# Optimization experiments

Hardware: AMD Instinct MI355X
Metric: run time of the kernel (lower is better)

The kernel has to match this reference:

```python
import jax, jax.numpy as jnp
import numpy as np

N_HEADS = 16


def _rope(q, k, freq_cos, freq_sin):
    # q,k: [B,S,H,hd]; freqs: [S, hd//2]
    B, S, H, hd = q.shape
    qr, qi = q.reshape(B, S, H, hd // 2, 2)[..., 0], q.reshape(B, S, H, hd // 2, 2)[..., 1]
    kr, ki = k.reshape(B, S, H, hd // 2, 2)[..., 0], k.reshape(B, S, H, hd // 2, 2)[..., 1]
    fc = freq_cos[None, :, None, :]  # [1,S,1,hd//2]
    fs = freq_sin[None, :, None, :]
    q_out = jnp.stack([qr * fc - qi * fs, qr * fs + qi * fc], axis=-1).reshape(B, S, H, hd)
    k_out = jnp.stack([kr * fc - ki * fs, kr * fs + ki * fc], axis=-1).reshape(B, S, H, hd)
    return q_out, k_out


def setup_inputs() -> dict:
    key = jax.random.key(0)
    ks = jax.random.split(key, 7)
    B, S, D = 2, 2048, 2048
    hd = D // N_HEADS
    scale = 1.0 / np.sqrt(D)
    return {
        "x": jax.random.normal(ks[0], (B, S, D), dtype=jnp.float32),
        "freq_cos": jnp.cos(jax.random.normal(ks[1], (S, hd // 2), dtype=jnp.float32)),
        "freq_sin": jnp.sin(jax.random.normal(ks[2], (S, hd // 2), dtype=jnp.float32)),
        "wq": jax.random.normal(ks[3], (D, D), dtype=jnp.float32) * scale,
        "wk": jax.random.normal(ks[4], (D, D), dtype=jnp.float32) * scale,
        "wv": jax.random.normal(ks[5], (D, D), dtype=jnp.float32) * scale,
        "wo": jax.random.normal(ks[6], (D, D), dtype=jnp.float32) * scale,
    }


def reference(x, freq_cos, freq_sin, wq, wk, wv, wo):
    B, S, D = x.shape
    H = N_HEADS
    hd = D // H
    # torch nn.Linear(weight [out,in]): y = x @ W^T
    q = (x @ wq.T).reshape(B, S, H, hd)
    k = (x @ wk.T).reshape(B, S, H, hd)
    v = (x @ wv.T).reshape(B, S, H, hd)
    q, k = _rope(q, k, freq_cos, freq_sin)
    # [B,H,S,hd]
    q = q.transpose(0, 2, 1, 3)
    k = k.transpose(0, 2, 1, 3)
    v = v.transpose(0, 2, 1, 3)
    scores = jnp.einsum("bhqd,bhkd->bhqk", q, k) / jnp.sqrt(jnp.float32(hd))
    causal = jnp.triu(jnp.full((S, S), -jnp.inf, dtype=scores.dtype), k=1)
    scores = scores + causal[None, None, :, :]
    probs = jax.nn.softmax(scores, axis=-1)
    out = jnp.einsum("bhqk,bhkd->bhqd", probs, v)
    out = out.transpose(0, 2, 1, 3).reshape(B, S, D)
    return out @ wo.T
```

## Files before the change

kernel.cpp:

```cpp
#include <hip/hip_runtime.h>
#include <hip/hip_bf16.h>
#include <stdint.h>

typedef unsigned short u16;
typedef unsigned int   u32;

typedef __attribute__((ext_vector_type(8))) short bf16x8;
typedef __attribute__((ext_vector_type(4))) float f32x4;
typedef __attribute__((ext_vector_type(4))) float f4;
typedef __attribute__((ext_vector_type(4))) u16   u16x4;

#define GLOBAL_AS __attribute__((address_space(1)))
#define LDS_AS    __attribute__((address_space(3)))

#define QSCALE (0.088388347648318447f * 1.4426950408889634f)

__device__ __forceinline__ void gload_lds16(const void* gsrc, void* ldst) {
    __builtin_amdgcn_global_load_lds((GLOBAL_AS const u32*)gsrc,
                                     (LDS_AS u32*)ldst, 16, 0, 0);
}

__device__ __forceinline__ float b2f(u16 u) {
    union { u32 i; float f; } x; x.i = ((u32)u) << 16; return x.f;
}
__device__ __forceinline__ u16 f2b(float f) {
    u32 u = __builtin_bit_cast(u32, f);
    u = (u + 0x7fff + ((u >> 16) & 1)) >> 16;
    return (u16)u;
}
__device__ __forceinline__ u16 f2b_tr(float f) {
    return (u16)(__builtin_bit_cast(u32, f) >> 16);
}

__global__ __launch_bounds__(256) void f2bf_kernel(const float* __restrict__ in,
                                                   u16* __restrict__ out, int n4) {
    int i = blockIdx.x * blockDim.x + threadIdx.x;
    if (i >= n4) return;
    f4 v = ((const f4*)in)[i];
    u16x4 o;
    o[0] = f2b(v[0]); o[1] = f2b(v[1]); o[2] = f2b(v[2]); o[3] = f2b(v[3]);
    ((u16x4*)out)[i] = o;
}

__global__ __launch_bounds__(256) void rope_kernel(u16* __restrict__ qkv,
                                                   const float* __restrict__ fc,
                                                   const float* __restrict__ fs) {
    const int S = 2048;
    int idx = blockIdx.x * blockDim.x + threadIdx.x;
    const int p   = idx & 1023;
    const int row = idx >> 10;
    const int s   = row & (S - 1);
    const int i   = p & 63;
    const float c = fc[s * 64 + i], sn = fs[s * 64 + i];
    u16* qa = qkv + (size_t)row * 6144 + p * 2;
    u16* ka = qa + 2048;
    u32 qq = *(const u32*)qa;
    float qr = b2f((u16)(qq & 0xffff)), qi = b2f((u16)(qq >> 16));
    u32 kk = *(const u32*)ka;
    float kr = b2f((u16)(kk & 0xffff)), ki = b2f((u16)(kk >> 16));
    u16 e0 = f2b(qr * c - qi * sn), e1 = f2b(qr * sn + qi * c);
    *(u32*)qa = (u32)e0 | ((u32)e1 << 16);
    e0 = f2b(kr * c - ki * sn); e1 = f2b(kr * sn + ki * c);
    *(u32*)ka = (u32)e0 | ((u32)e1 << 16);
}

template<int OUT_MODE>
__global__ __launch_bounds__(512, 2)
void gemm_bt(const u16* __restrict__ A, const u16* __restrict__ B,
             void* __restrict__ Cptr, int M, int N, int Kdim) {
    __shared__ char lds[3][49152];
    const int t = threadIdx.x, l = t & 63, w = t >> 6;
    const int g = l >> 4, r16 = l & 15;

    const int nwg = gridDim.x * gridDim.y;
    const int id  = blockIdx.y * gridDim.x + blockIdx.x;
    const int swz = (id & 7) * (nwg >> 3) + (id >> 3);
    const int bx  = swz % gridDim.x, by = swz / gridDim.x;
    const int m0 = by * 256, n0 = bx * 128;
    const int wm = w >> 1, wn = w & 1;
    const int rA = wm * 64, rB = wn * 64;

    f32x4 acc[4][4];
#pragma unroll
    for (int i = 0; i < 4; i++)
#pragma unroll
        for (int j = 0; j < 4; j++) acc[i][j] = (f32x4){0.f, 0.f, 0.f, 0.f};

    const int nk = Kdim >> 6;

    auto stage = [&](int kt, int bi) {
        const int k0 = kt << 6;
#pragma unroll
        for (int q = 0; q < 4; q++) {
            const int o = q * 8192 + w * 1024 + l * 16;
            const int row = o >> 7;
            const int cb = (o & 127) ^ ((row & 7) << 4);
            gload_lds16(A + (size_t)(m0 + row) * Kdim + k0 + (cb >> 1),
                        &lds[bi][q * 8192 + w * 1024]);
        }
#pragma unroll
        for (int q = 0; q < 2; q++) {
            const int o = q * 8192 + w * 1024 + l * 16;
            const int row = o >> 7;
            const int cb = (o & 127) ^ ((row & 7) << 4);
            gload_lds16(B + (size_t)(n0 + row) * Kdim + k0 + (cb >> 1),
                        &lds[bi][32768 + q * 8192 + w * 1024]);
        }
    };

    stage(0, 0);
    stage(1, 1);

    for (int kt = 0; kt < nk; ++kt) {
        const int cur = kt % 3;
        __builtin_amdgcn_sched_barrier(0);
        __builtin_amdgcn_s_barrier();
        stage((kt + 2) % nk, (kt + 2) % 3);
        asm volatile("s_waitcnt vmcnt(12)" ::: "memory");
        __builtin_amdgcn_s_barrier();
        __builtin_amdgcn_sched_barrier(0);

        const char* Ab = lds[cur];
        const char* Bb = lds[cur] + 32768;
        bf16x8 af[2][4], bfr[2][4];
#pragma unroll
        for (int kk = 0; kk < 2; kk++)
#pragma unroll
            for (int i = 0; i < 4; i++) {
                const int rowa = rA + i * 16 + r16;
                const int cba = (kk * 64 + g * 16) ^ ((rowa & 7) << 4);
                af[kk][i] = *(const bf16x8*)(Ab + rowa * 128 + cba);
                const int rowb = rB + i * 16 + r16;
                const int cbb = (kk * 64 + g * 16) ^ ((rowb & 7) << 4);
                bfr[kk][i] = *(const bf16x8*)(Bb + rowb * 128 + cbb);
            }
#pragma unroll
        for (int kk = 0; kk < 2; kk++)
#pragma unroll
            for (int mi = 0; mi < 4; mi++)
#pragma unroll
                for (int ni = 0; ni < 4; ni++)
                    acc[mi][ni] = __builtin_amdgcn_mfma_f32_16x16x32_bf16(af[kk][mi],
                                                                          bfr[kk][ni],
                                                                          acc[mi][ni], 0, 0, 0);
    }

#pragma unroll
    for (int mi = 0; mi < 4; mi++)
#pragma unroll
        for (int ni = 0; ni < 4; ni++)
#pragma unroll
            for (int r = 0; r < 4; r++) {
                int row = m0 + rA + mi * 16 + g * 4 + r;
                int col = n0 + rB + ni * 16 + r16;
                float v = acc[mi][ni][r];
                if (OUT_MODE == 0)      ((float*)Cptr)[(size_t)row * N + col] = v;
                else if (OUT_MODE == 1) ((u16*)Cptr)[(size_t)row * N + col] = f2b(v);
                else ((u16*)Cptr)[(size_t)row * N + col] =
                         f2b(col < 2048 ? v * QSCALE : v);
            }
}

__global__ __launch_bounds__(512, 2)
void flash_attn(const u16* __restrict__ QKV, u16* __restrict__ Op) {
    const int S = 2048, DQ = 6144, DO = 2048;
    __shared__ u16 klds[2][128 * 128];
    __shared__ u16 vtlds[128 * 136];
    __shared__ u16 plds[8][16 * 136];
    const int t = threadIdx.x, l = t & 63, w = t >> 6;
    const int g = l >> 4, r16 = l & 15;
    const int bh = blockIdx.x, b = bh >> 4, h = bh & 15;
    const size_t base = ((size_t)(b * S)) * DQ + h * 128;
    const u16* qp = QKV + base;
    const u16* kp = qp + 2048;
    const u16* vp = qp + 4096;
    const size_t obase = ((size_t)(b * S)) * DO + h * 128;

    for (int task = 0; task < 2; ++task) {
        const int tq = task ? (15 - (int)blockIdx.y) : (int)blockIdx.y;
        const int q0 = tq * 128;
        const int nkt = tq + 1;

        bf16x8 qf[4];
#pragma unroll
        for (int ks = 0; ks < 4; ks++)
            qf[ks] = *(const bf16x8*)(qp + (size_t)(q0 + w * 16 + r16) * DQ
                                      + ks * 32 + g * 8);

        f32x4 acc[8];
#pragma unroll
        for (int i = 0; i < 8; i++) acc[i] = (f32x4){0.f, 0.f, 0.f, 0.f};
        float m_run[4], s_run[4];
#pragma unroll
        for (int r = 0; r < 4; r++) { m_run[r] = -3.0e38f; s_run[r] = 0.f; }

        auto stageK = [&](int bi, int kv0) {
#pragma unroll
            for (int i = 0; i < 4; i++) {
                const int o = (w * 4 + i) * 1024 + l * 16;
                const int row = o >> 8;
                const int cb = (o & 255) ^ ((row & 7) << 4);
                gload_lds16(kp + (size_t)(kv0 + row) * DQ + (cb >> 1),
                            (char*)klds[bi] + (w * 4 + i) * 1024);
            }
        };
        bf16x8 vv[2][2];
        auto loadV = [&](int kv0) {
#pragma unroll
            for (int c = 0; c < 2; c++)
#pragma unroll
                for (int kh = 0; kh < 2; kh++)
                    vv[c][kh] = *(const bf16x8*)(vp + (size_t)(kv0 + kh * 64 + l) * DQ
                                                 + (w * 16 + c * 8));
        };
        auto writeVT = [&]() {
#pragma unroll
            for (int c = 0; c < 2; c++)
#pragma unroll
                for (int kh = 0; kh < 2; kh++) {
                    const int d0 = w * 16 + c * 8;
#pragma unroll
                    for (int j = 0; j < 8; j++)
                        vtlds[(d0 + j) * 136 + kh * 64 + l] = (u16)vv[c][kh][j];
                }
        };

        stageK(0, 0);
        loadV(0);
        __syncthreads();
        writeVT();
        __syncthreads();

        int cur = 0;
        for (int kt = 0; kt < nkt; ++kt) {
            const int kv0 = kt * 128;
            const bool more = (kt + 1 < nkt);
            if (more) { stageK(cur ^ 1, kv0 + 128); loadV(kv0 + 128); }

            f32x4 sf[8];
#pragma unroll
            for (int nf = 0; nf < 8; nf++) sf[nf] = (f32x4){0.f, 0.f, 0.f, 0.f};
#pragma unroll
            for (int nf = 0; nf < 8; nf++) {
                const int row = nf * 16 + r16;
                const int rb = row * 256;
#pragma unroll
                for (int ks = 0; ks < 4; ks++) {
                    const int cb = (ks * 64 + g * 16) ^ ((row & 7) << 4);
                    bf16x8 kf = *(const bf16x8*)((const char*)klds[cur] + rb + cb);
                    sf[nf] = __builtin_amdgcn_mfma_f32_16x16x32_bf16(qf[ks], kf,
                                                                     sf[nf], 0, 0, 0);
                }
            }

            const bool diag = (kt == tq);
            float mt[4];
#pragma unroll
            for (int r = 0; r < 4; r++) mt[r] = -3.0e38f;
#pragma unroll
            for (int nf = 0; nf < 8; nf++)
#pragma unroll
                for (int r = 0; r < 4; r++) {
                    float s = sf[nf][r];
                    if (diag) {
                        int qrow = q0 + w * 16 + g * 4 + r;
                        int kcol = kv0 + nf * 16 + r16;
                        if (kcol > qrow) s = -3.0e38f;
                    }
                    sf[nf][r] = s;
                    mt[r] = fmaxf(mt[r], s);
                }
#pragma unroll
            for (int r = 0; r < 4; r++) {
#pragma unroll
                for (int d = 1; d < 16; d <<= 1)
                    mt[r] = fmaxf(mt[r], __shfl_xor(mt[r], d));
            }
            int grow = (mt[0] > m_run[0] + 8.f) | (mt[1] > m_run[1] + 8.f) |
                       (mt[2] > m_run[2] + 8.f) | (mt[3] > m_run[3] + 8.f);
            if (__any(grow)) {
#pragma unroll
                for (int r = 0; r < 4; r++) {
                    float mn = fmaxf(m_run[r], mt[r]);
                    float alpha = exp2f(m_run[r] - mn);
                    m_run[r] = mn;
                    s_run[r] *= alpha;
#pragma unroll
                    for (int i = 0; i < 8; i++) acc[i][r] *= alpha;
                }
            }
            float psum[4];
#pragma unroll
            for (int r = 0; r < 4; r++) psum[r] = 0.f;
#pragma unroll
            for (int nf = 0; nf < 8; nf++)
#pragma unroll
                for (int r = 0; r < 4; r++) {
                    float p = exp2f(sf[nf][r] - m_run[r]);
                    psum[r] += p;
                    plds[w][(g * 4 + r) * 136 + nf * 16 + r16] = f2b_tr(p);
                }
#pragma unroll
            for (int r = 0; r < 4; r++) {
#pragma unroll
                for (int d = 1; d < 16; d <<= 1)
                    psum[r] += __shfl_xor(psum[r], d);
                s_run[r] += psum[r];
            }
            __builtin_amdgcn_s_setprio(1);
#pragma unroll
            for (int ks2 = 0; ks2 < 4; ks2++) {
                bf16x8 pf = *(const bf16x8*)(&plds[w][r16 * 136 + ks2 * 32 + g * 8]);
#pragma unroll
                for (int nf8 = 0; nf8 < 8; nf8++) {
                    bf16x8 vf = *(const bf16x8*)(&vtlds[(nf8 * 16 + r16) * 136
                                                         + ks2 * 32 + g * 8]);
                    acc[nf8] = __builtin_amdgcn_mfma_f32_16x16x32_bf16(pf, vf,
                                                                       acc[nf8], 0, 0, 0);
                }
            }
            __builtin_amdgcn_s_setprio(0);

            __syncthreads();
            if (more) writeVT();
            __syncthreads();
            cur ^= 1;
        }

        float inv[4];
#pragma unroll
        for (int r = 0; r < 4; r++) inv[r] = 1.0f / s_run[r];
#pragma unroll
        for (int nf8 = 0; nf8 < 8; nf8++)
#pragma unroll
            for (int r = 0; r < 4; r++) {
                size_t idx = obase + (size_t)(q0 + w * 16 + g * 4 + r) * DO
                             + nf8 * 16 + r16;
                Op[idx] = f2b(acc[nf8][r] * inv[r]);
            }
    }
}

extern "C" void kernel_launch(void* const* d_in, const int* in_sizes, int n_in,
                              void* d_out, int out_size, void* d_ws, size_t ws_size,
                              hipStream_t stream) {
    const float* x  = (const float*)d_in[0];
    const float* fc = (const float*)d_in[1];
    const float* fs = (const float*)d_in[2];
    const float* wq = (const float*)d_in[3];
    const float* wk = (const float*)d_in[4];
    const float* wv = (const float*)d_in[5];
    const float* wo = (const float*)d_in[6];
    float* out = (float*)d_out;

    const int S = 2048, D = 2048;
    const int M = 2 * S;
    const size_t MD = (size_t)M * D;
    const size_t DD = (size_t)D * D;

    u16* xb   = (u16*)d_ws;
    u16* wqb  = xb  + MD;
    u16* wkb  = wqb + DD;
    u16* wvb  = wkb + DD;
    u16* wob  = wvb + DD;
    u16* qkvb = wob + DD;

    f2bf_kernel<<<(int)(MD / 1024), 256, 0, stream>>>(x,  xb,  (int)(MD / 4));
    f2bf_kernel<<<(int)(DD / 1024), 256, 0, stream>>>(wq, wqb, (int)(DD / 4));
    f2bf_kernel<<<(int)(DD / 1024), 256, 0, stream>>>(wk, wkb, (int)(DD / 4));
    f2bf_kernel<<<(int)(DD / 1024), 256, 0, stream>>>(wv, wvb, (int)(DD / 4));
    f2bf_kernel<<<(int)(DD / 1024), 256, 0, stream>>>(wo, wob, (int)(DD / 4));

    gemm_bt<2><<<dim3(6144 / 128, M / 256), 512, 0, stream>>>(xb, wqb, qkvb, M, 6144, D);

    rope_kernel<<<(int)(MD / 2 / 256), 256, 0, stream>>>(qkvb, fc, fs);

    flash_attn<<<dim3(32, 8), 512, 0, stream>>>(qkvb, xb);

    gemm_bt<0><<<dim3(D / 128, M / 256), 512, 0, stream>>>(xb, wob, out, M, D, D);
}
```

Measured before the change: 285.9 us.

## Add 256x256 eight-phase pipelined GEMM for the fused QKV projection

Adds a new GEMM kernel using 256x256 output tiles with 8 waves. It splits each K-step into quadrant phases that interleave LDS reads, async global-to-LDS loads and MFMA blocks, separated by barriers and priority hints. The kernel is used only for the QKV projection; the output projection still uses the old kernel. Larger tiles raise data reuse and the staged schedule is meant to hide load latency. The cost is 128KB of LDS per block, which limits occupancy, plus many barriers. The k-index wrap with nk-1 assumes K is a power of two.

```diff
diff --git a/kernel.cpp b/kernel.cpp
--- a/kernel.cpp
+++ b/kernel.cpp
@@ -64,6 +64,142 @@
     *(u32*)ka = (u32)e0 | ((u32)e1 << 16);
 }
 
+#define BAR8() do { __builtin_amdgcn_sched_barrier(0); \
+                    __builtin_amdgcn_s_barrier();      \
+                    __builtin_amdgcn_sched_barrier(0); } while (0)
+
+template<int OUT_MODE>
+__global__ __launch_bounds__(512, 2)
+void gemm8(const u16* __restrict__ A, const u16* __restrict__ B,
+           void* __restrict__ Cptr, int M, int N, int Kdim) {
+    __shared__ char lds[131072];
+    const int t = threadIdx.x, l = t & 63, w = t >> 6;
+    const int g = l >> 4, r16 = l & 15;
+    const int wm = w >> 2, wn = w & 3;
+
+    const int nwg = gridDim.x * gridDim.y;
+    const int id  = blockIdx.y * gridDim.x + blockIdx.x;
+    const int swz = (id & 7) * (nwg >> 3) + (id >> 3);
+    const int bx  = swz % gridDim.x, by = swz / gridDim.x;
+    const int m0 = by * 256, n0 = bx * 256;
+
+    f32x4 acc[8][4];
+#pragma unroll
+    for (int i = 0; i < 8; i++)
+#pragma unroll
+        for (int j = 0; j < 4; j++) acc[i][j] = (f32x4){0.f, 0.f, 0.f, 0.f};
+
+    const int sw  = (r16 & 7) << 4;
+    const int cK0 = (g * 16) ^ sw;
+    const int cK1 = (64 + g * 16) ^ sw;
+
+    bf16x8 afA[4][2], bfA[2][2], bfB[2][2];
+
+    auto stgA = [&](int d, int r, int kt) {
+#pragma unroll
+        for (int i = 0; i < 2; i++) {
+            const int o  = (i * 8 + w) * 1024 + l * 16;
+            const int rr = o >> 7;
+            const int cb = (o & 127) ^ ((rr & 7) << 4);
+            const int gr = ((rr >> 6) << 7) + r * 64 + (rr & 63);
+            gload_lds16(A + (size_t)(m0 + gr) * Kdim + kt * 64 + (cb >> 1),
+                        lds + d * 65536 + r * 16384 + (i * 8 + w) * 1024);
+        }
+    };
+    auto stgB = [&](int d, int r, int kt) {
+#pragma unroll
+        for (int i = 0; i < 2; i++) {
+            const int o  = (i * 8 + w) * 1024 + l * 16;
+            const int rr = o >> 7;
+            const int cb = (o & 127) ^ ((rr & 7) << 4);
+            const int gc = ((rr >> 5) << 6) + r * 32 + (rr & 31);
+            gload_lds16(B + (size_t)(n0 + gc) * Kdim + kt * 64 + (cb >> 1),
+                        lds + d * 65536 + 32768 + r * 16384 + (i * 8 + w) * 1024);
+        }
+    };
+    auto rdA = [&](int d, int qm) {
+#pragma unroll
+        for (int mi = 0; mi < 4; mi++) {
+            const char* p = lds + d * 65536 + qm * 16384
+                            + (wm * 64 + mi * 16 + r16) * 128;
+            afA[mi][0] = *(const bf16x8*)(p + cK0);
+            afA[mi][1] = *(const bf16x8*)(p + cK1);
+        }
+    };
+    auto rdB = [&](bf16x8 (&dst)[2][2], int d, int qn) {
+#pragma unroll
+        for (int ni = 0; ni < 2; ni++) {
+            const char* p = lds + d * 65536 + 32768 + qn * 16384
+                            + (wn * 32 + ni * 16 + r16) * 128;
+            dst[ni][0] = *(const bf16x8*)(p + cK0);
+            dst[ni][1] = *(const bf16x8*)(p + cK1);
+        }
+    };
+    auto mm = [&](int qm, int qn, bf16x8 (&bf)[2][2]) {
+        __builtin_amdgcn_s_setprio(1);
+#pragma unroll
+        for (int kk = 0; kk < 2; kk++)
+#pragma unroll
+            for (int mi = 0; mi < 4; mi++)
+#pragma unroll
+                for (int ni = 0; ni < 2; ni++)
+                    acc[qm * 4 + mi][qn * 2 + ni] =
+                        __builtin_amdgcn_mfma_f32_16x16x32_bf16(
+                            afA[mi][kk], bf[ni][kk],
+                            acc[qm * 4 + mi][qn * 2 + ni], 0, 0, 0);
+        __builtin_amdgcn_s_setprio(0);
+    };
+
+    const int nk = Kdim >> 6;
+
+    stgA(0, 0, 0); stgB(0, 1, 0); stgB(0, 0, 0); stgA(0, 1, 0);
+    stgA(1, 0, 1); stgB(1, 1, 1);
+    asm volatile("s_waitcnt vmcnt(4)" ::: "memory");
+    BAR8();
+
+    for (int tt = 0; tt < (nk >> 1); ++tt) {
+        const int b1 = (2 * tt + 1);
+        const int a2 = (2 * tt + 2) & (nk - 1);
+        const int b2 = (2 * tt + 3) & (nk - 1);
+
+        rdA(0, 0); rdB(bfA, 0, 0); stgB(1, 0, b1); BAR8();
+        mm(0, 0, bfA); BAR8();
+        rdB(bfB, 0, 1); stgA(1, 1, b1); BAR8();
+        mm(0, 1, bfB); BAR8();
+        rdA(0, 1); stgA(0, 0, a2); BAR8();
+        mm(1, 1, bfB); BAR8();
+        stgB(0, 1, a2); BAR8();
+        mm(1, 0, bfA);
+        asm volatile("s_waitcnt vmcnt(4)" ::: "memory");
+        BAR8();
+        rdA(1, 0); rdB(bfA, 1, 0); stgB(0, 0, a2); BAR8();
+        mm(0, 0, bfA); BAR8();
+        rdB(bfB, 1, 1); stgA(0, 1, a2); BAR8();
+        mm(0, 1, bfB); BAR8();
+        rdA(1, 1); stgA(1, 0, b2); BAR8();
+        mm(1, 1, bfB); BAR8();
+        stgB(1, 1, b2); BAR8();
+        mm(1, 0, bfA);
+        asm volatile("s_waitcnt vmcnt(4)" ::: "memory");
+        BAR8();
+    }
+
+#pragma unroll
+    for (int a = 0; a < 8; a++)
+#pragma unroll
+        for (int b = 0; b < 4; b++)
+#pragma unroll
+            for (int r = 0; r < 4; r++) {
+                int row = m0 + wm * 128 + a * 16 + g * 4 + r;
+                int col = n0 + wn * 64 + b * 16 + r16;
+                float v = acc[a][b][r];
+                if (OUT_MODE == 0)      ((float*)Cptr)[(size_t)row * N + col] = v;
+                else if (OUT_MODE == 1) ((u16*)Cptr)[(size_t)row * N + col] = f2b(v);
+                else ((u16*)Cptr)[(size_t)row * N + col] =
+                         f2b(col < 2048 ? v * QSCALE : v);
+            }
+}
+
 template<int OUT_MODE>
 __global__ __launch_bounds__(512, 2)
 void gemm_bt(const u16* __restrict__ A, const u16* __restrict__ B,
@@ -371,7 +507,7 @@
     f2bf_kernel<<<(int)(DD / 1024), 256, 0, stream>>>(wv, wvb, (int)(DD / 4));
     f2bf_kernel<<<(int)(DD / 1024), 256, 0, stream>>>(wo, wob, (int)(DD / 4));
 
-    gemm_bt<2><<<dim3(6144 / 128, M / 256), 512, 0, stream>>>(xb, wqb, qkvb, M, 6144, D);
+    gemm8<2><<<dim3(6144 / 256, M / 256), 512, 0, stream>>>(xb, wqb, qkvb, M, 6144, D);
 
     rope_kernel<<<(int)(MD / 2 / 256), 256, 0, stream>>>(qkvb, fc, fs);
 
```

New measurement: 286.7 us. No clear change (+0.3%).
